# Kernel tuning notes

Hardware: AMD Instinct MI355X
Metric: run time of the kernel (lower is better)

Reference implementation:

```python
import jax, jax.numpy as jnp
import numpy as np

DISCRETE_VALUES = jnp.array([-1.0, 0.0, 1.0], dtype=jnp.float32)  # sorted, D=3


def setup_inputs() -> dict:
    key = jax.random.key(0)
    k1, k2, k3 = jax.random.split(key, 3)
    n, in_feat, out_feat, D = 2048, 4096, 4096, 3
    x = jax.random.normal(k1, (n, in_feat), dtype=jnp.float32)
    W_logits = jax.random.normal(k2, (D, out_feat, in_feat), dtype=jnp.float32)
    b_logits = jax.random.normal(k3, (D, out_feat, 1), dtype=jnp.float32)
    return {"x": x, "W_logits": W_logits, "b_logits": b_logits}


def _gaussian_dist_parameters(logits, values):
    # softmax over the discrete-value axis (axis 0) -> per-weight distribution
    p = jax.nn.softmax(logits, axis=0)            # (D, out, in)
    mean = jnp.einsum("d,doi->oi", values, p)      # E[w]
    sq = jnp.einsum("d,doi->oi", values * values, p)  # E[w^2]
    var = sq - mean * mean                          # Var[w]
    return mean, var


def reference(x, W_logits, b_logits):
    vals = DISCRETE_VALUES
    w_mean, w_var = _gaussian_dist_parameters(W_logits, vals)  # (out, in)
    # REAL input branch: out_mean = w_mean @ x^T ; out_var = w_var @ (x^2)^T
    out_mean = jnp.einsum("oi,ni->no", w_mean, x)              # (n, out)
    out_var = jnp.einsum("oi,ni->no", w_var, x * x)            # (n, out)
    # LOGIT bias: add bias distribution moments
    b_mean, b_var = _gaussian_dist_parameters(b_logits, vals)  # (out, 1)
    out_mean = out_mean + b_mean[:, 0]
    out_var = out_var + b_var[:, 0]
    return jnp.stack([out_mean, out_var], axis=1)              # (n, 2, out)
```

## Files before the change

kernel.cpp:

```cpp
#include <hip/hip_runtime.h>

#define NROWS 2048
#define NOUT  4096
#define NIN   4096

#define BM 128
#define BN 128
#define BK 128

#define SX   (6.0f / 127.0f)
#define SX2  (36.0f / 127.0f)
#define SW   (1.0f / 127.0f)

typedef __attribute__((ext_vector_type(4))) int i32x4;

__device__ __forceinline__ char q8(float v, float inv_s) {
    float q = rintf(v * inv_s);
    q = fmaxf(-127.f, fminf(127.f, q));
    return (char)(int)q;
}

__global__ __launch_bounds__(256) void prep_kernel(
        const float* __restrict__ Wl,
        const float* __restrict__ x,
        char* __restrict__ wmq,
        char* __restrict__ wvq,
        char* __restrict__ xq,
        char* __restrict__ x2q) {
    const int bid = blockIdx.x;
    if (bid < 16384) {
        const long long total = (long long)NOUT * NIN;
        const long long idx = ((long long)bid * 256 + threadIdx.x) * 4;
        float4 l0 = *(const float4*)(Wl + idx);
        float4 l1 = *(const float4*)(Wl + total + idx);
        float4 l2 = *(const float4*)(Wl + 2 * total + idx);
        float a0[4] = {l0.x, l0.y, l0.z, l0.w};
        float a1[4] = {l1.x, l1.y, l1.z, l1.w};
        float a2[4] = {l2.x, l2.y, l2.z, l2.w};
        char mo[4], vo[4];
#pragma unroll
        for (int j = 0; j < 4; ++j) {
            float e0 = __expf(a0[j]);
            float e1 = __expf(a1[j]);
            float e2 = __expf(a2[j]);
            float inv = 1.0f / (e0 + e1 + e2);
            float mean = (e2 - e0) * inv;
            float sq   = (e2 + e0) * inv;
            float var  = fmaf(-mean, mean, sq);
            mo[j] = q8(mean, 127.0f);
            vo[j] = q8(var, 127.0f);
        }
        *(char4*)(wmq + idx) = make_char4(mo[0], mo[1], mo[2], mo[3]);
        *(char4*)(wvq + idx) = make_char4(vo[0], vo[1], vo[2], vo[3]);
    } else {
        const long long idx = ((long long)(bid - 16384) * 256 + threadIdx.x) * 4;
        float4 v = *(const float4*)(x + idx);
        float a[4] = {v.x, v.y, v.z, v.w};
        char xo[4], x2o[4];
#pragma unroll
        for (int j = 0; j < 4; ++j) {
            xo[j]  = q8(a[j], 127.0f / 6.0f);
            x2o[j] = q8(a[j] * a[j], 127.0f / 36.0f);
        }
        *(char4*)(xq + idx)  = make_char4(xo[0], xo[1], xo[2], xo[3]);
        *(char4*)(x2q + idx) = make_char4(x2o[0], x2o[1], x2o[2], x2o[3]);
    }
}

__global__ __launch_bounds__(256, 4) void gemm_moments_kernel(
        const char* __restrict__ xq,
        const char* __restrict__ x2q,
        const char* __restrict__ wmq,
        const char* __restrict__ wvq,
        const float* __restrict__ blogits,
        float* __restrict__ out) {
    __shared__ __align__(16) char sA[BM * BK];
    __shared__ __align__(16) char sB[BN * BK];

    const int z = blockIdx.z;
    const char* __restrict__ Ab = z ? x2q : xq;
    const char* __restrict__ Wb = z ? wvq : wmq;

    const int m0 = blockIdx.y * BM;
    const int o0 = blockIdx.x * BN;
    const int tid  = threadIdx.x;
    const int lane = tid & 63;
    const int wave = tid >> 6;
    const int wm = wave >> 1;
    const int wn = wave & 1;

    const int r_in = lane >> 3;
    const int g_f  = (lane & 7) ^ r_in;
    const int cB   = g_f * 16;

    unsigned offA[4], offB[4];
#pragma unroll
    for (int t = 0; t < 4; ++t) {
        const int q = wave * 4 + t;
        offA[t] = (unsigned)((m0 + q * 8 + r_in) * NIN + cB);
        offB[t] = (unsigned)((o0 + q * 8 + r_in) * NIN + cB);
    }

    i32x4 acc[4][4];
#pragma unroll
    for (int i = 0; i < 4; ++i)
#pragma unroll
        for (int j = 0; j < 4; ++j) acc[i][j] = (i32x4){0, 0, 0, 0};

    const int quad = lane >> 4;
    const int mr   = lane & 15;

    for (int k0 = 0; k0 < NIN; k0 += BK) {
#pragma unroll
        for (int t = 0; t < 4; ++t) {
            const int q = wave * 4 + t;
            __builtin_amdgcn_global_load_lds(
                (const __attribute__((address_space(1))) void*)(Ab + offA[t]),
                (__attribute__((address_space(3))) void*)(sA + q * (8 * BK)),
                16, 0, 0);
            __builtin_amdgcn_global_load_lds(
                (const __attribute__((address_space(1))) void*)(Wb + offB[t]),
                (__attribute__((address_space(3))) void*)(sB + q * (8 * BK)),
                16, 0, 0);
            offA[t] += BK;
            offB[t] += BK;
        }
        __syncthreads();

#pragma unroll
        for (int ks = 0; ks < 2; ++ks) {
            i32x4 afrag[4], bfrag[4];
#pragma unroll
            for (int t = 0; t < 4; ++t) {
                const int ra = wm * 64 + t * 16 + mr;
                const int rb = wn * 64 + t * 16 + mr;
                const int slot = (ks * 4 + quad) ^ (mr & 7);
                afrag[t] = *(const i32x4*)(sA + ra * BK + slot * 16);
                bfrag[t] = *(const i32x4*)(sB + rb * BK + slot * 16);
            }
#pragma unroll
            for (int tm = 0; tm < 4; ++tm)
#pragma unroll
                for (int tn = 0; tn < 4; ++tn)
                    acc[tm][tn] = __builtin_amdgcn_mfma_i32_16x16x64_i8(
                        afrag[tm], bfrag[tn], acc[tm][tn], 0, 0, 0);
        }
        __syncthreads();
    }

    const float oscale = z ? (SX2 * SW) : (SX * SW);
    const int cn = lane & 15;
#pragma unroll
    for (int tn = 0; tn < 4; ++tn) {
        const int o = o0 + wn * 64 + tn * 16 + cn;
        float l0 = blogits[o];
        float l1 = blogits[NOUT + o];
        float l2 = blogits[2 * NOUT + o];
        float e0 = __expf(l0), e1 = __expf(l1), e2 = __expf(l2);
        float inv = 1.0f / (e0 + e1 + e2);
        float bm = (e2 - e0) * inv;
        float bias = z ? fmaf(-bm, bm, (e2 + e0) * inv) : bm;
#pragma unroll
        for (int tm = 0; tm < 4; ++tm) {
            const int mb = m0 + wm * 64 + tm * 16 + quad * 4;
            float* op = out + (long long)mb * (2 * NOUT) + (long long)z * NOUT + o;
#pragma unroll
            for (int r = 0; r < 4; ++r) {
                op[(long long)r * (2 * NOUT)] = fmaf((float)acc[tm][tn][r], oscale, bias);
            }
        }
    }
}

extern "C" void kernel_launch(void* const* d_in, const int* in_sizes, int n_in,
                              void* d_out, int out_size, void* d_ws, size_t ws_size,
                              hipStream_t stream) {
    const float* x  = (const float*)d_in[0];
    const float* Wl = (const float*)d_in[1];
    const float* bl = (const float*)d_in[2];
    float* out = (float*)d_out;

    char* ws = (char*)d_ws;
    char* wmq = ws;
    char* wvq = ws + 16777216;
    char* xq  = ws + 33554432;
    char* x2q = ws + 41943040;

    prep_kernel<<<24576, 256, 0, stream>>>(Wl, x, wmq, wvq, xq, x2q);

    dim3 grid(NOUT / BN, NROWS / BM, 2);
    gemm_moments_kernel<<<grid, 256, 0, stream>>>(xq, x2q, wmq, wvq, bl, out);
}
```

Before: 378.9 us.

## Restructure int8 GEMM into 256x256 tiles with multi-stage LDS pipelining

The int8 MFMA GEMM moves from 128x128 tiles with 4 waves and a single LDS buffer to 256x256 tiles with 8 waves. LDS is now double-buffered per k-half, and asynchronous global-to-LDS loads are issued ahead, gated by explicit vmcnt waits and barriers. Compute phases are raised with s_setprio and interleaved with staging. The goal is to overlap global loads with MFMA work and raise arithmetic intensity per block. In exchange it uses far more LDS and registers (128 accumulator VGPRs per lane), and the grid shrinks to 256 blocks, which may underfill the GPU.

```diff
diff --git a/kernel.cpp b/kernel.cpp
--- a/kernel.cpp
+++ b/kernel.cpp
@@ -4,15 +4,14 @@
 #define NOUT  4096
 #define NIN   4096
 
-#define BM 128
-#define BN 128
-#define BK 128
-
 #define SX   (6.0f / 127.0f)
 #define SX2  (36.0f / 127.0f)
 #define SW   (1.0f / 127.0f)
 
 typedef __attribute__((ext_vector_type(4))) int i32x4;
+
+#define AS1 __attribute__((address_space(1)))
+#define AS3 __attribute__((address_space(3)))
 
 __device__ __forceinline__ char q8(float v, float inv_s) {
     float q = rintf(v * inv_s);
@@ -67,92 +66,164 @@
     }
 }
 
-__global__ __launch_bounds__(256, 4) void gemm_moments_kernel(
+
+#define NT 32
+
+#define NOSTG ((void)0)
+#define NOWT  ((void)0)
+#define WAIT8 asm volatile("s_waitcnt vmcnt(8)" ::: "memory")
+#define WAIT4 asm volatile("s_waitcnt vmcnt(4)" ::: "memory")
+#define WAIT0 asm volatile("s_waitcnt vmcnt(0)" ::: "memory")
+
+#define STAGE(GPTR, OFF, SBASE, pp, kss, koff)                                  \
+    do {                                                                        \
+        __builtin_amdgcn_global_load_lds(                                       \
+            (const AS1 void*)((GPTR) + (OFF)[0] + (koff)),                      \
+            (AS3 void*)((SBASE) + ((pp) * 2 + (kss)) * 16384 + wave * 1024),    \
+            16, 0, 0);                                                          \
+        __builtin_amdgcn_global_load_lds(                                       \
+            (const AS1 void*)((GPTR) + (OFF)[1] + (koff)),                      \
+            (AS3 void*)((SBASE) + ((pp) * 2 + (kss)) * 16384 + 8192 +           \
+                        wave * 1024),                                           \
+            16, 0, 0);                                                          \
+    } while (0)
+
+#define MFMA_BLOCK(QB)                                                          \
+    _Pragma("unroll")                                                           \
+    for (int nt_ = 0; nt_ < 4; ++nt_) {                                         \
+        _Pragma("unroll")                                                       \
+        for (int mt_ = 0; mt_ < 4; ++mt_) {                                     \
+            acc[(QB) + mt_][nt_] = __builtin_amdgcn_mfma_i32_16x16x64_i8(       \
+                af[mt_], bf[nt_], acc[(QB) + mt_][nt_], 0, 0, 0);               \
+        }                                                                       \
+    }
+
+#define PH_Q0(pp, kss, STG, WT)                                                 \
+    {                                                                           \
+        const char* sAk = sA + ((pp) * 2 + (kss)) * 16384;                      \
+        const char* sBk = sB + ((pp) * 2 + (kss)) * 16384;                      \
+        af[0] = *(const i32x4*)(sAk + aoffb);                                   \
+        af[1] = *(const i32x4*)(sAk + aoffb + 1024);                            \
+        af[2] = *(const i32x4*)(sAk + aoffb + 2048);                            \
+        af[3] = *(const i32x4*)(sAk + aoffb + 3072);                            \
+        bf[0] = *(const i32x4*)(sBk + boffb);                                   \
+        bf[1] = *(const i32x4*)(sBk + boffb + 1024);                            \
+        bf[2] = *(const i32x4*)(sBk + boffb + 2048);                            \
+        bf[3] = *(const i32x4*)(sBk + boffb + 3072);                            \
+        STG;                                                                    \
+        WT;                                                                     \
+        __builtin_amdgcn_s_barrier();                                           \
+        __builtin_amdgcn_s_setprio(1);                                          \
+        MFMA_BLOCK(0);                                                          \
+        __builtin_amdgcn_s_setprio(0);                                          \
+        __builtin_amdgcn_s_barrier();                                           \
+    }
+
+#define PH_Q1(pp, kss, STG, WT)                                                 \
+    {                                                                           \
+        const char* sAk = sA + ((pp) * 2 + (kss)) * 16384;                      \
+        af[0] = *(const i32x4*)(sAk + aoffb + 4096);                            \
+        af[1] = *(const i32x4*)(sAk + aoffb + 5120);                            \
+        af[2] = *(const i32x4*)(sAk + aoffb + 6144);                            \
+        af[3] = *(const i32x4*)(sAk + aoffb + 7168);                            \
+        STG;                                                                    \
+        WT;                                                                     \
+        __builtin_amdgcn_s_barrier();                                           \
+        __builtin_amdgcn_s_setprio(1);                                          \
+        MFMA_BLOCK(4);                                                          \
+        __builtin_amdgcn_s_setprio(0);                                          \
+        __builtin_amdgcn_s_barrier();                                           \
+    }
+
+#define KTILE(pp, S1, S2, S3, S4, W2, W4)                                       \
+    PH_Q0(pp, 0, S1, NOWT)                                                      \
+    PH_Q1(pp, 0, S2, W2)                                                        \
+    PH_Q0(pp, 1, S3, NOWT)                                                      \
+    PH_Q1(pp, 1, S4, W4)
+
+__global__ __launch_bounds__(512, 2) void gemm_moments_kernel(
         const char* __restrict__ xq,
         const char* __restrict__ x2q,
         const char* __restrict__ wmq,
         const char* __restrict__ wvq,
         const float* __restrict__ blogits,
         float* __restrict__ out) {
-    __shared__ __align__(16) char sA[BM * BK];
-    __shared__ __align__(16) char sB[BN * BK];
+    __shared__ __align__(16) char sA[2 * 2 * 16384];
+    __shared__ __align__(16) char sB[2 * 2 * 16384];
 
     const int z = blockIdx.z;
     const char* __restrict__ Ab = z ? x2q : xq;
     const char* __restrict__ Wb = z ? wvq : wmq;
 
-    const int m0 = blockIdx.y * BM;
-    const int o0 = blockIdx.x * BN;
+    const int m0 = blockIdx.y * 256;
+    const int o0 = blockIdx.x * 256;
     const int tid  = threadIdx.x;
     const int lane = tid & 63;
     const int wave = tid >> 6;
-    const int wm = wave >> 1;
-    const int wn = wave & 1;
-
-    const int r_in = lane >> 3;
-    const int g_f  = (lane & 7) ^ r_in;
-    const int cB   = g_f * 16;
-
-    unsigned offA[4], offB[4];
-#pragma unroll
-    for (int t = 0; t < 4; ++t) {
-        const int q = wave * 4 + t;
-        offA[t] = (unsigned)((m0 + q * 8 + r_in) * NIN + cB);
-        offB[t] = (unsigned)((o0 + q * 8 + r_in) * NIN + cB);
-    }
-
-    i32x4 acc[4][4];
-#pragma unroll
-    for (int i = 0; i < 4; ++i)
-#pragma unroll
-        for (int j = 0; j < 4; ++j) acc[i][j] = (i32x4){0, 0, 0, 0};
+    const int wm = wave >> 2;
+    const int wn = wave & 3;
 
     const int quad = lane >> 4;
     const int mr   = lane & 15;
-
-    for (int k0 = 0; k0 < NIN; k0 += BK) {
-#pragma unroll
-        for (int t = 0; t < 4; ++t) {
-            const int q = wave * 4 + t;
-            __builtin_amdgcn_global_load_lds(
-                (const __attribute__((address_space(1))) void*)(Ab + offA[t]),
-                (__attribute__((address_space(3))) void*)(sA + q * (8 * BK)),
-                16, 0, 0);
-            __builtin_amdgcn_global_load_lds(
-                (const __attribute__((address_space(1))) void*)(Wb + offB[t]),
-                (__attribute__((address_space(3))) void*)(sB + q * (8 * BK)),
-                16, 0, 0);
-            offA[t] += BK;
-            offB[t] += BK;
-        }
-        __syncthreads();
-
-#pragma unroll
-        for (int ks = 0; ks < 2; ++ks) {
-            i32x4 afrag[4], bfrag[4];
-#pragma unroll
-            for (int t = 0; t < 4; ++t) {
-                const int ra = wm * 64 + t * 16 + mr;
-                const int rb = wn * 64 + t * 16 + mr;
-                const int slot = (ks * 4 + quad) ^ (mr & 7);
-                afrag[t] = *(const i32x4*)(sA + ra * BK + slot * 16);
-                bfrag[t] = *(const i32x4*)(sB + rb * BK + slot * 16);
-            }
-#pragma unroll
-            for (int tm = 0; tm < 4; ++tm)
-#pragma unroll
-                for (int tn = 0; tn < 4; ++tn)
-                    acc[tm][tn] = __builtin_amdgcn_mfma_i32_16x16x64_i8(
-                        afrag[tm], bfrag[tn], acc[tm][tn], 0, 0, 0);
-        }
-        __syncthreads();
-    }
+    const int swz  = (quad ^ ((mr >> 1) & 3)) * 16;
+    const int aoffb = (wm * 128 + mr) * 64 + swz;
+    const int boffb = (wn * 64 + mr) * 64 + swz;
+
+    const int srow = tid >> 2;
+    const int sg   = (tid & 3) ^ ((tid >> 3) & 3);
+    unsigned offA[2], offB[2];
+#pragma unroll
+    for (int i = 0; i < 2; ++i) {
+        offA[i] = (unsigned)((m0 + i * 128 + srow) * NIN + sg * 16);
+        offB[i] = (unsigned)((o0 + i * 128 + srow) * NIN + sg * 16);
+    }
+
+    i32x4 acc[8][4];
+#pragma unroll
+    for (int i = 0; i < 8; ++i)
+#pragma unroll
+        for (int j = 0; j < 4; ++j) acc[i][j] = (i32x4){0, 0, 0, 0};
+    i32x4 af[4];
+    i32x4 bf[4];
+
+    STAGE(Ab, offA, sA, 0, 0, 0);
+    STAGE(Wb, offB, sB, 0, 0, 0);
+    STAGE(Ab, offA, sA, 0, 1, 64);
+    STAGE(Wb, offB, sB, 0, 1, 64);
+    STAGE(Ab, offA, sA, 1, 0, 128);
+    STAGE(Wb, offB, sB, 1, 0, 128);
+    WAIT8;
+    __builtin_amdgcn_s_barrier();
+
+#pragma unroll 1
+    for (int t = 0; t < NT - 2; t += 2) {
+        const int kb = t * 128;
+        KTILE(0,
+              STAGE(Ab, offA, sA, 1, 1, kb + 192),
+              STAGE(Wb, offB, sB, 1, 1, kb + 192),
+              STAGE(Ab, offA, sA, 0, 0, kb + 256),
+              STAGE(Wb, offB, sB, 0, 0, kb + 256),
+              WAIT8, WAIT8);
+        KTILE(1,
+              STAGE(Ab, offA, sA, 0, 1, kb + 320),
+              STAGE(Wb, offB, sB, 0, 1, kb + 320),
+              STAGE(Ab, offA, sA, 1, 0, kb + 384),
+              STAGE(Wb, offB, sB, 1, 0, kb + 384),
+              WAIT8, WAIT8);
+    }
+
+    KTILE(0,
+          STAGE(Ab, offA, sA, 1, 1, 4032),
+          STAGE(Wb, offB, sB, 1, 1, 4032),
+          NOSTG, NOSTG,
+          WAIT8, WAIT4);
+    KTILE(1, NOSTG, NOSTG, NOSTG, NOSTG, WAIT0, NOWT);
 
     const float oscale = z ? (SX2 * SW) : (SX * SW);
     const int cn = lane & 15;
 #pragma unroll
-    for (int tn = 0; tn < 4; ++tn) {
-        const int o = o0 + wn * 64 + tn * 16 + cn;
+    for (int nt = 0; nt < 4; ++nt) {
+        const int o = o0 + wn * 64 + nt * 16 + cn;
         float l0 = blogits[o];
         float l1 = blogits[NOUT + o];
         float l2 = blogits[2 * NOUT + o];
@@ -161,12 +232,13 @@
         float bm = (e2 - e0) * inv;
         float bias = z ? fmaf(-bm, bm, (e2 + e0) * inv) : bm;
 #pragma unroll
-        for (int tm = 0; tm < 4; ++tm) {
-            const int mb = m0 + wm * 64 + tm * 16 + quad * 4;
+        for (int mt = 0; mt < 8; ++mt) {
+            const int mb = m0 + wm * 128 + mt * 16 + quad * 4;
             float* op = out + (long long)mb * (2 * NOUT) + (long long)z * NOUT + o;
 #pragma unroll
             for (int r = 0; r < 4; ++r) {
-                op[(long long)r * (2 * NOUT)] = fmaf((float)acc[tm][tn][r], oscale, bias);
+                op[(long long)r * (2 * NOUT)] =
+                    fmaf((float)acc[mt][nt][r], oscale, bias);
             }
         }
     }
@@ -188,6 +260,6 @@
 
     prep_kernel<<<24576, 256, 0, stream>>>(Wl, x, wmq, wvq, xq, x2q);
 
-    dim3 grid(NOUT / BN, NROWS / BM, 2);
-    gemm_moments_kernel<<<grid, 256, 0, stream>>>(xq, x2q, wmq, wvq, bl, out);
-}
+    dim3 grid(NOUT / 256, NROWS / 256, 2);
+    gemm_moments_kernel<<<grid, 512, 0, stream>>>(xq, x2q, wmq, wvq, bl, out);
+}
```

After: 376.9 us. No clear change (-0.5%).
